# Performance work log

Hardware: AMD Instinct MI355X
Metric: run time of the kernel (lower is better)

## Reference

```python
import jax, jax.numpy as jnp
import numpy as np

CE_W, DICE_W, BD_W = 1.0, 3.0, 2.0   # combined-loss lambdas
BPW = 10.0                            # boundary pixel weight
SMOOTH = 1e-6                         # dice smoothing
# cv2.getStructuringElement(cv2.MORPH_ELLIPSE, (5,5))
ELLIPSE5 = np.array([[0,0,1,0,0],
                     [1,1,1,1,1],
                     [1,1,1,1,1],
                     [1,1,1,1,1],
                     [0,0,1,0,0]], dtype=bool)


def setup_inputs() -> dict:
    key = jax.random.key(0)
    k1, k2 = jax.random.split(key)
    B, C, H, W = 8, 8, 512, 1024
    pred = jax.random.normal(k1, (B, C, H, W), dtype=jnp.float32)
    target = jax.random.randint(k2, (B, H, W), 0, C).astype(jnp.int32)
    return {"pred": pred, "target": target}


def _morph(mask, is_dilate):
    """Grayscale dilate/erode with 5x5 ellipse SE (matches cv2 default border:
    padding value never wins the max/min)."""
    pad_val = 0 if is_dilate else jnp.iinfo(jnp.int32).max
    p = jnp.pad(mask, ((0, 0), (2, 2), (2, 2)), constant_values=pad_val)
    H, W = mask.shape[1], mask.shape[2]
    out = None
    for dy in range(5):
        for dx in range(5):
            if not ELLIPSE5[dy, dx]:
                continue
            s = p[:, dy:dy + H, dx:dx + W]
            if out is None:
                out = s
            else:
                out = jnp.maximum(out, s) if is_dilate else jnp.minimum(out, s)
    return out


def reference(pred, target):
    B, C, H, W = pred.shape
    logp = jax.nn.log_softmax(pred, axis=1)                         # (B,C,H,W)
    # per-pixel cross entropy
    ce_map = -jnp.take_along_axis(logp, target[:, None], axis=1)[:, 0]  # (B,H,W)
    ce = ce_map.mean()
    # dice over softmax probs vs one-hot target
    probs = jnp.exp(logp)
    onehot = jax.nn.one_hot(target, C, dtype=pred.dtype, axis=1)    # (B,C,H,W)
    inter = jnp.sum(probs * onehot, axis=(2, 3))                    # (B,C)
    card = jnp.sum(probs, axis=(2, 3)) + jnp.sum(onehot, axis=(2, 3))
    dice = 1.0 - jnp.mean((2.0 * inter + SMOOTH) / (card + SMOOTH))
    # boundary mask = morphological gradient of the label map
    t = target.astype(jnp.int32)
    boundary = _morph(t, True) - _morph(t, False)                   # (B,H,W)
    wmap = jnp.where(boundary > 0, jnp.float32(BPW), jnp.float32(1.0))
    bd = jnp.mean(ce_map * wmap)
    return CE_W * ce + DICE_W * dice + BD_W * bd
```

## Files before the change

kernel.cpp:

```cpp
#include <hip/hip_runtime.h>
#include <math.h>

constexpr int B = 8, C = 8, H = 512, W = 1024;
constexpr int TW = 64, TH = 16;
constexpr int BX = 64, BY = 4;
constexpr int HALO = 2;
constexpr int LW = TW + 2 * HALO;
constexpr int LH = TH + 2 * HALO;
constexpr float BPW = 10.0f;
constexpr float SMOOTH = 1e-6f;

constexpr int ACC_N = 2 + 3 * B * C;

__global__ __launch_bounds__(BX * BY)
void loss_main(const float* __restrict__ pred, const int* __restrict__ target,
               float* __restrict__ acc) {
    __shared__ int smask[LH][LW];
    __shared__ float sred[4][26];

    const int tx = threadIdx.x, ty = threadIdx.y;
    const int tid = ty * BX + tx;
    const int w0 = blockIdx.x * TW;
    const int h0 = blockIdx.y * TH;
    const int b  = blockIdx.z;

    const int* tb = target + (size_t)b * H * W;
    for (int i = tid; i < LH * LW; i += BX * BY) {
        int ly = i / LW, lx = i % LW;
        int gh = h0 - HALO + ly, gw = w0 - HALO + lx;
        int m = 0;
        if (gh >= 0 && gh < H && gw >= 0 && gw < W) m = 1 << tb[gh * W + gw];
        smask[ly][lx] = m;
    }
    __syncthreads();

    float ce_s = 0.f, bd_s = 0.f;
    float p_s[C], in_s[C], ct_s[C];
#pragma unroll
    for (int c = 0; c < C; ++c) { p_s[c] = 0.f; in_s[c] = 0.f; ct_s[c] = 0.f; }

    const size_t plane = (size_t)H * W;
    const float* pb = pred + (size_t)b * C * plane;

#pragma unroll
    for (int r = 0; r < TH / BY; ++r) {
        const int y = ty + r * BY;
        const int h = h0 + y;
        const int w = w0 + tx;
        const size_t pix = (size_t)h * W + w;

        float x[C];
#pragma unroll
        for (int c = 0; c < C; ++c) x[c] = pb[c * plane + pix];

        float m = x[0];
#pragma unroll
        for (int c = 1; c < C; ++c) m = fmaxf(m, x[c]);

        float e[C];
        float s = 0.f;
#pragma unroll
        for (int c = 0; c < C; ++c) { e[c] = __expf(x[c] - m); s += e[c]; }

        const int cm = smask[y + HALO][tx + HALO];
        const int t = 31 - __clz(cm);

        float xt = x[0];
#pragma unroll
        for (int c = 1; c < C; ++c) xt = (t == c) ? x[c] : xt;

        const float lse = m + __logf(s);
        const float ce = lse - xt;

        int bm = cm;
        bm |= smask[y + 0][tx + 2];
#pragma unroll
        for (int dx = 0; dx < 5; ++dx) {
            bm |= smask[y + 1][tx + dx];
            bm |= smask[y + 2][tx + dx];
            bm |= smask[y + 3][tx + dx];
        }
        bm |= smask[y + 4][tx + 2];

        const float wgt = (bm & (bm - 1)) ? BPW : 1.f;
        ce_s += ce;
        bd_s += ce * wgt;

        const float invs = 1.f / s;
#pragma unroll
        for (int c = 0; c < C; ++c) {
            const float p = e[c] * invs;
            p_s[c] += p;
            const bool is_t = (c == t);
            in_s[c] += is_t ? p : 0.f;
            ct_s[c] += is_t ? 1.f : 0.f;
        }
    }

    float vals[26];
    vals[0] = ce_s; vals[1] = bd_s;
#pragma unroll
    for (int c = 0; c < C; ++c) {
        vals[2 + c] = p_s[c];
        vals[10 + c] = in_s[c];
        vals[18 + c] = ct_s[c];
    }
#pragma unroll
    for (int k = 0; k < 26; ++k) {
        float v = vals[k];
#pragma unroll
        for (int off = 32; off > 0; off >>= 1) v += __shfl_down(v, off, 64);
        vals[k] = v;
    }
    const int lane = tid & 63, wid = tid >> 6;
    if (lane == 0) {
#pragma unroll
        for (int k = 0; k < 26; ++k) sred[wid][k] = vals[k];
    }
    __syncthreads();
    if (tid < 26) {
        const float v = sred[0][tid] + sred[1][tid] + sred[2][tid] + sred[3][tid];
        int gi;
        if (tid == 0)       gi = 0;
        else if (tid == 1)  gi = 1;
        else if (tid < 10)  gi = 2 + b * C + (tid - 2);
        else if (tid < 18)  gi = 2 + B * C + b * C + (tid - 10);
        else                gi = 2 + 2 * B * C + b * C + (tid - 18);
        atomicAdd(&acc[gi], v);
    }
}

__global__ void loss_final(const float* __restrict__ acc, float* __restrict__ out) {
    const int i = threadIdx.x;
    const float psum  = acc[2 + i];
    const float inter = acc[2 + B * C + i];
    const float cnt   = acc[2 + 2 * B * C + i];
    float d = (2.f * inter + SMOOTH) / (psum + cnt + SMOOTH);
#pragma unroll
    for (int off = 32; off > 0; off >>= 1) d += __shfl_down(d, off, 64);
    if (i == 0) {
        const float N = (float)B * H * W;
        const float ce = acc[0] / N;
        const float bd = acc[1] / N;
        const float dice = 1.f - d / (float)(B * C);
        out[0] = 1.0f * ce + 3.0f * dice + 2.0f * bd;
    }
}

extern "C" void kernel_launch(void* const* d_in, const int* in_sizes, int n_in,
                              void* d_out, int out_size, void* d_ws, size_t ws_size,
                              hipStream_t stream) {
    const float* pred = (const float*)d_in[0];
    const int* target = (const int*)d_in[1];
    float* acc = (float*)d_ws;
    float* out = (float*)d_out;

    hipMemsetAsync(acc, 0, ACC_N * sizeof(float), stream);

    dim3 grid(W / TW, H / TH, B);
    dim3 block(BX, BY, 1);
    loss_main<<<grid, block, 0, stream>>>(pred, target, acc);
    loss_final<<<1, 64, 0, stream>>>(acc, out);
}
```

Measured before the change: 234.4 us.

## Vectorize pred loads as float4 and pack label masks into bytes

Each thread now handles four adjacent pixels, loading the logits with float4 reads, and the tile widens to 256x8. The label one-hot masks are packed four per 32-bit word in shared memory, so the 5x5 boundary stencil becomes a few word reads plus byte extraction instead of many scalar shared loads. The aim is fewer memory instructions and less shared-memory traffic for this bandwidth-bound pass. In exchange each thread uses more registers for 32 logits, and the halo staging does scalar global loads with byte packing.

New measurement: 217.1 us. -7.4%, faster.

```diff
diff --git a/kernel.cpp b/kernel.cpp
--- a/kernel.cpp
+++ b/kernel.cpp
@@ -2,20 +2,24 @@
 #include <math.h>
 
 constexpr int B = 8, C = 8, H = 512, W = 1024;
-constexpr int TW = 64, TH = 16;
+constexpr int TW = 256, TH = 8;
 constexpr int BX = 64, BY = 4;
 constexpr int HALO = 2;
-constexpr int LW = TW + 2 * HALO;
 constexpr int LH = TH + 2 * HALO;
+constexpr int LWD = 66;
 constexpr float BPW = 10.0f;
 constexpr float SMOOTH = 1e-6f;
 
 constexpr int ACC_N = 2 + 3 * B * C;
 
+__device__ __forceinline__ unsigned byte_of(unsigned lo, unsigned hi, int k) {
+    return (k < 4) ? ((lo >> (8 * k)) & 0xFFu) : ((hi >> (8 * (k - 4))) & 0xFFu);
+}
+
 __global__ __launch_bounds__(BX * BY)
 void loss_main(const float* __restrict__ pred, const int* __restrict__ target,
                float* __restrict__ acc) {
-    __shared__ int smask[LH][LW];
+    __shared__ unsigned smask[LH][LWD];
     __shared__ float sred[4][26];
 
     const int tx = threadIdx.x, ty = threadIdx.y;
@@ -25,12 +29,21 @@
     const int b  = blockIdx.z;
 
     const int* tb = target + (size_t)b * H * W;
-    for (int i = tid; i < LH * LW; i += BX * BY) {
-        int ly = i / LW, lx = i % LW;
-        int gh = h0 - HALO + ly, gw = w0 - HALO + lx;
-        int m = 0;
-        if (gh >= 0 && gh < H && gw >= 0 && gw < W) m = 1 << tb[gh * W + gw];
-        smask[ly][lx] = m;
+
+    for (int i = tid; i < LH * LWD; i += BX * BY) {
+        const int row = i / LWD, dw = i % LWD;
+        const int gh = h0 - HALO + row;
+        unsigned pack = 0u;
+        if (gh >= 0 && gh < H) {
+            const int gbase = w0 - HALO + dw * 4;
+#pragma unroll
+            for (int k = 0; k < 4; ++k) {
+                const int gw = gbase + k;
+                const unsigned v = (gw >= 0 && gw < W) ? (1u << tb[gh * W + gw]) : 0u;
+                pack |= v << (8 * k);
+            }
+        }
+        smask[row][dw] = pack;
     }
     __syncthreads();
 
@@ -46,54 +59,68 @@
     for (int r = 0; r < TH / BY; ++r) {
         const int y = ty + r * BY;
         const int h = h0 + y;
-        const int w = w0 + tx;
-        const size_t pix = (size_t)h * W + w;
+        const int wbase = w0 + tx * 4;
+        const size_t pix = (size_t)h * W + wbase;
 
-        float x[C];
+        float4 xv[C];
 #pragma unroll
-        for (int c = 0; c < C; ++c) x[c] = pb[c * plane + pix];
+        for (int c = 0; c < C; ++c)
+            xv[c] = *reinterpret_cast<const float4*>(pb + c * plane + pix);
 
-        float m = x[0];
+        const unsigned r1lo = smask[y + 1][tx], r1hi = smask[y + 1][tx + 1];
+        const unsigned r2lo = smask[y + 2][tx], r2hi = smask[y + 2][tx + 1];
+        const unsigned r3lo = smask[y + 3][tx], r3hi = smask[y + 3][tx + 1];
+        const unsigned t0lo = smask[y + 0][tx], t0hi = smask[y + 0][tx + 1];
+        const unsigned t4lo = smask[y + 4][tx], t4hi = smask[y + 4][tx + 1];
+        const unsigned rlo = r1lo | r2lo | r3lo, rhi = r1hi | r2hi | r3hi;
+
+        unsigned wb[8];
 #pragma unroll
-        for (int c = 1; c < C; ++c) m = fmaxf(m, x[c]);
+        for (int k = 0; k < 8; ++k) wb[k] = byte_of(rlo, rhi, k);
 
-        float e[C];
-        float s = 0.f;
-#pragma unroll
-        for (int c = 0; c < C; ++c) { e[c] = __expf(x[c] - m); s += e[c]; }
-
-        const int cm = smask[y + HALO][tx + HALO];
-        const int t = 31 - __clz(cm);
-
-        float xt = x[0];
-#pragma unroll
-        for (int c = 1; c < C; ++c) xt = (t == c) ? x[c] : xt;
-
-        const float lse = m + __logf(s);
-        const float ce = lse - xt;
-
-        int bm = cm;
-        bm |= smask[y + 0][tx + 2];
-#pragma unroll
-        for (int dx = 0; dx < 5; ++dx) {
-            bm |= smask[y + 1][tx + dx];
-            bm |= smask[y + 2][tx + dx];
-            bm |= smask[y + 3][tx + dx];
-        }
-        bm |= smask[y + 4][tx + 2];
-
-        const float wgt = (bm & (bm - 1)) ? BPW : 1.f;
-        ce_s += ce;
-        bd_s += ce * wgt;
-
-        const float invs = 1.f / s;
+        float xs[4][C];
 #pragma unroll
         for (int c = 0; c < C; ++c) {
-            const float p = e[c] * invs;
-            p_s[c] += p;
-            const bool is_t = (c == t);
-            in_s[c] += is_t ? p : 0.f;
-            ct_s[c] += is_t ? 1.f : 0.f;
+            xs[0][c] = xv[c].x; xs[1][c] = xv[c].y; xs[2][c] = xv[c].z; xs[3][c] = xv[c].w;
+        }
+
+#pragma unroll
+        for (int j = 0; j < 4; ++j) {
+            const unsigned cm = byte_of(r2lo, r2hi, 2 + j);
+            const int t = 31 - __clz(cm);
+
+            unsigned bm = wb[j] | wb[j + 1] | wb[j + 2] | wb[j + 3] | wb[j + 4];
+            bm |= byte_of(t0lo, t0hi, 2 + j) | byte_of(t4lo, t4hi, 2 + j);
+
+            const float m01 = fmaxf(xs[j][0], xs[j][1]);
+            const float m23 = fmaxf(xs[j][2], xs[j][3]);
+            const float m45 = fmaxf(xs[j][4], xs[j][5]);
+            const float m67 = fmaxf(xs[j][6], xs[j][7]);
+            const float m = fmaxf(fmaxf(m01, m23), fmaxf(m45, m67));
+
+            float e[C];
+#pragma unroll
+            for (int c = 0; c < C; ++c) e[c] = __expf(xs[j][c] - m);
+            const float s = ((e[0] + e[1]) + (e[2] + e[3])) + ((e[4] + e[5]) + (e[6] + e[7]));
+
+            float xt = xs[j][0];
+#pragma unroll
+            for (int c = 1; c < C; ++c) xt = (t == c) ? xs[j][c] : xt;
+
+            const float ce = (m + __logf(s)) - xt;
+            const float wgt = (bm & (bm - 1)) ? BPW : 1.f;
+            ce_s += ce;
+            bd_s += ce * wgt;
+
+            const float invs = 1.f / s;
+#pragma unroll
+            for (int c = 0; c < C; ++c) {
+                const float p = e[c] * invs;
+                p_s[c] += p;
+                const bool is_t = (c == t);
+                in_s[c] += is_t ? p : 0.f;
+                ct_s[c] += is_t ? 1.f : 0.f;
+            }
         }
     }
 
```
